# Kernel tuning notes

Hardware: AMD Instinct MI355X
Metric: run time of the kernel (lower is better)

The kernel has to match this reference:

```python
import jax, jax.numpy as jnp
import numpy as np

N_HEADS = 16


def _rotate_half(x):
    x_even = x[..., ::2]
    x_odd = x[..., 1::2]
    return jnp.stack((-x_odd, x_even), axis=-1).reshape(x.shape)


def _apply_rope(x, cos, sin):
    # cos/sin: (S, d_head) broadcast against (B, H, S, d_head)
    return x * cos + _rotate_half(x) * sin


def setup_inputs() -> dict:
    key = jax.random.key(0)
    k1, k2, k3 = jax.random.split(key, 3)
    B, S, D, H = 2, 2048, 1024, N_HEADS
    dh = D // H
    x = jax.random.normal(k1, (B, S, D), dtype=jnp.float32)
    w_qkv = jax.random.normal(k2, (D, 3 * D), dtype=jnp.float32) * 0.02
    w_proj = jax.random.normal(k3, (D, D), dtype=jnp.float32) * 0.02
    # standard interleaved RoPE tables, shape (S, d_head)
    inv_freq = 1.0 / (10000.0 ** (jnp.arange(0, dh, 2, dtype=jnp.float32) / dh))
    angles = jnp.arange(S, dtype=jnp.float32)[:, None] * inv_freq[None, :]  # (S, dh/2)
    rope_cos = jnp.repeat(jnp.cos(angles), 2, axis=-1)  # (S, dh)
    rope_sin = jnp.repeat(jnp.sin(angles), 2, axis=-1)
    return {"x": x, "w_qkv": w_qkv, "w_proj": w_proj, "rope_cos": rope_cos, "rope_sin": rope_sin}


def reference(x, w_qkv, w_proj, rope_cos, rope_sin):
    B, S, D = x.shape
    H = N_HEADS
    dh = D // H
    half = dh // 2
    qkv = x @ w_qkv  # (B, S, 3D)
    q, k, v = jnp.split(qkv, 3, axis=-1)
    # (B, S, D) -> (B, H, S, dh)
    q = q.reshape(B, S, H, dh).transpose(0, 2, 1, 3)
    k = k.reshape(B, S, H, dh).transpose(0, 2, 1, 3)
    v = v.reshape(B, S, H, dh).transpose(0, 2, 1, 3)
    q = _apply_rope(q, rope_cos, rope_sin)
    k = _apply_rope(k, rope_cos, rope_sin)
    scale = half ** -0.5
    # dual score matrices from the two half-subspaces
    attn_up = jnp.einsum('bhid,bhjd->bhij', q[..., :half], k[..., :half]) * scale
    attn_down = jnp.einsum('bhid,bhjd->bhij', q[..., half:], k[..., half:]) * scale
    lower_mask = jnp.tril(jnp.ones((S, S), dtype=bool))  # j <= i -> down
    attn_logits = jnp.where(lower_mask, attn_down, attn_up)
    attn_weights = jax.nn.softmax(attn_logits, axis=-1)
    attn_out = jnp.einsum('bhij,bhjd->bhid', attn_weights, v)
    attn_out = attn_out.transpose(0, 2, 1, 3).reshape(B, S, D)
    return attn_out @ w_proj
```

## Files before the change

### kernel.cpp

```cpp
#include <hip/hip_runtime.h>
#include <hip/hip_bf16.h>
#include <stdint.h>

typedef __bf16 bf16;
typedef __attribute__((ext_vector_type(4))) __bf16 bf16x4;
typedef __attribute__((ext_vector_type(8))) __bf16 bf16x8;
typedef __attribute__((ext_vector_type(4))) float f32x4;

#define MFMA16(a, b, c) __builtin_amdgcn_mfma_f32_16x16x32_bf16((a), (b), (c), 0, 0, 0)

#define QSC (0.17677669529663687f * 1.4426950408889634f)

__device__ __forceinline__ void async_cp16(const bf16* g, bf16* l) {
  __builtin_amdgcn_global_load_lds(
      (const __attribute__((address_space(1))) void*)g,
      (__attribute__((address_space(3))) void*)l, 16, 0, 0);
}

__global__ __launch_bounds__(256) void prep_k(const float* __restrict__ x,
                                              bf16* __restrict__ xb,
                                              const float* __restrict__ wqkv,
                                              bf16* __restrict__ wqkvT,
                                              const float* __restrict__ wproj,
                                              bf16* __restrict__ wprojT) {
  __shared__ bf16 t[64][65];
  const int bid = blockIdx.x;
  if (bid < 1024) {
    int i = (bid * 256 + threadIdx.x) * 4;
    const int stride = 1024 * 256 * 4;
    for (; i < 4194304; i += stride) {
      const f32x4 f = *(const f32x4*)(x + i);
      bf16x4 o;
      o[0] = (bf16)f[0]; o[1] = (bf16)f[1]; o[2] = (bf16)f[2]; o[3] = (bf16)f[3];
      *(bf16x4*)(xb + i) = o;
    }
    return;
  }
  const float* in;
  bf16* out;
  int R, C, tb;
  if (bid < 1792) { in = wqkv; out = wqkvT; R = 1024; C = 3072; tb = bid - 1024; }
  else            { in = wproj; out = wprojT; R = 1024; C = 1024; tb = bid - 1792; }
  const int tilesx = C >> 6;
  const int bc = (tb % tilesx) * 64, br = (tb / tilesx) * 64;
  const int tx = threadIdx.x & 63, ty = threadIdx.x >> 6;
#pragma unroll
  for (int r = ty; r < 64; r += 4) t[r][tx] = (bf16)in[(br + r) * C + bc + tx];
  __syncthreads();
#pragma unroll
  for (int r = ty; r < 64; r += 4) out[(bc + r) * R + br + tx] = t[tx][r];
}

template <int MODE, int BM>
__global__ __launch_bounds__(256) void gemm128(
    const bf16* __restrict__ A, const bf16* __restrict__ BT, int M, int N, int K,
    float* __restrict__ C, bf16* __restrict__ qws, bf16* __restrict__ kws,
    bf16* __restrict__ vT, const float* __restrict__ ropeC, const float* __restrict__ ropeS) {
  constexpr int MT = BM / 32;
  __shared__ __align__(16) bf16 As[BM * 64];
  __shared__ __align__(16) bf16 Bs[128 * 64];
  const int tid = threadIdx.x;
  const int lane = tid & 63, wave = tid >> 6;
  const int l16 = lane & 15, quad = lane >> 4;
  const int wm = (wave >> 1) * (BM / 2), wn = (wave & 1) * 64;
  const int bm = blockIdx.y, bn = blockIdx.x;

  const int srow = tid >> 3;
  const int schunk = ((tid & 7) - srow) & 7;
  const bf16* ag = A + (bm * BM + srow) * K + schunk * 8;
  const bf16* bg = BT + (bn * 128 + srow) * K + schunk * 8;
  bf16* la = &As[tid * 8];
  bf16* lb = &Bs[tid * 8];

  f32x4 acc[MT][4] = {};

  for (int k0 = 0; k0 < K; k0 += 64) {
    async_cp16(ag + k0, la);
    async_cp16(ag + 32 * K + k0, la + 2048);
    if (BM == 128) {
      async_cp16(ag + 64 * K + k0, la + 4096);
      async_cp16(ag + 96 * K + k0, la + 6144);
    }
    async_cp16(bg + k0, lb);
    async_cp16(bg + 32 * K + k0, lb + 2048);
    async_cp16(bg + 64 * K + k0, lb + 4096);
    async_cp16(bg + 96 * K + k0, lb + 6144);
    __syncthreads();
#pragma unroll
    for (int ks = 0; ks < 2; ++ks) {
      bf16x8 af[MT], bff[4];
#pragma unroll
      for (int t = 0; t < MT; ++t) {
        const int r = wm + t * 16 + l16;
        af[t] = *(const bf16x8*)&As[r * 64 + ((ks * 4 + quad + r) & 7) * 8];
      }
#pragma unroll
      for (int t = 0; t < 4; ++t) {
        const int r = wn + t * 16 + l16;
        bff[t] = *(const bf16x8*)&Bs[r * 64 + ((ks * 4 + quad + r) & 7) * 8];
      }
#pragma unroll
      for (int mt = 0; mt < MT; ++mt)
#pragma unroll
        for (int nt = 0; nt < 4; ++nt) acc[mt][nt] = MFMA16(af[mt], bff[nt], acc[mt][nt]);
    }
    __syncthreads();
  }

  if (MODE == 0) {
#pragma unroll
    for (int mt = 0; mt < MT; ++mt)
#pragma unroll
      for (int i = 0; i < 4; ++i) {
        const int row = bm * BM + wm + mt * 16 + quad * 4 + i;
#pragma unroll
        for (int nt = 0; nt < 4; ++nt) {
          const int col = bn * 128 + wn + nt * 16 + l16;
          C[row * N + col] = acc[mt][nt][i];
        }
      }
  } else {
    bf16* tb = &Bs[wave * 512];
#pragma unroll
    for (int mt = 0; mt < MT; ++mt) {
      const int s0 = bm * BM + wm + mt * 16;
      const int b = s0 >> 11, sbase = s0 & 2047;
#pragma unroll
      for (int nt = 0; nt < 4; ++nt) {
        const int colb = bn * 128 + wn + nt * 16;
        const int sec = colb >> 10, rem = colb & 1023;
        const int h = rem >> 6, d0 = rem & 63;
        if (sec < 2) {
          const int d = d0 + l16;
#pragma unroll
          for (int i = 0; i < 4; ++i) {
            const int s = sbase + quad * 4 + i;
            float v = acc[mt][nt][i];
            float pr = __shfl_xor(v, 1);
            float rot = (d & 1) ? pr : -pr;
            float rv = v * ropeC[s * 64 + d] + rot * ropeS[s * 64 + d];
            if (sec == 0) rv *= QSC;
            tb[(quad * 4 + i) * 20 + l16] = (bf16)rv;
          }
          bf16* dst = ((sec == 0) ? qws : kws) + ((b * 16 + h) * 2048 + sbase) * 64 + d0;
          bf16x4 seg = *(const bf16x4*)&tb[l16 * 20 + quad * 4];
          *(bf16x4*)(dst + l16 * 64 + quad * 4) = seg;
        } else {
          const int d = d0 + l16;
          const int s4 = sbase + quad * 4;
          const int a = (s4 >> 4) & 3;
          const int p = (s4 & ~63) | ((a >> 1) * 32 + quad * 8 + (a & 1) * 4);
          bf16x4 pk;
#pragma unroll
          for (int i = 0; i < 4; ++i) pk[i] = (bf16)acc[mt][nt][i];
          *(bf16x4*)(vT + ((b * 16 + h) * 64 + d) * 2048 + p) = pk;
        }
      }
    }
  }
}

template <int SPLIT>
__global__ __launch_bounds__(256) void attn_k(const bf16* __restrict__ qws,
                                              const bf16* __restrict__ kws,
                                              const bf16* __restrict__ vT,
                                              bf16* __restrict__ awA, bf16* __restrict__ pB,
                                              float* __restrict__ lA, float* __restrict__ lB) {
  __shared__ __align__(16) bf16 Ks[2][64 * 64];
  __shared__ __align__(16) bf16 Vs[2][64 * 64];
  const int tid = threadIdx.x;
  const int lane = tid & 63, wave = tid >> 6;
  const int l16 = lane & 15, quad = lane >> 4;
  int bh, qblk, kh;
  if (SPLIT) {
    bh = blockIdx.x & 31;
    const int q2 = blockIdx.x >> 5;
    qblk = q2 >> 1;
    kh = q2 & 1;
  } else {
    bh = blockIdx.x >> 4;
    qblk = blockIdx.x & 15;
    kh = 0;
  }
  const int b = bh >> 4, h = bh & 15;
  const int rbase = qblk * 128 + wave * 32;
  const int jt0 = kh * 16;
  const int jt1 = SPLIT ? jt0 + 16 : 32;

  const bf16* qb = qws + (bh * 2048 + rbase) * 64;
  const bf16* kb = kws + bh * 2048 * 64;
  const bf16* vb = vT + bh * 64 * 2048;

  const int r0 = wave * 16 + (lane >> 3);
  const int c0 = ((lane & 7) - r0) & 7;
  const bf16* kst0 = kb + r0 * 64 + c0 * 8;
  const bf16* kst1 = kb + (r0 + 8) * 64 + c0 * 8;
  const bf16* vst0 = vb + r0 * 2048 + c0 * 8;
  const bf16* vst1 = vb + (r0 + 8) * 2048 + c0 * 8;

#define STAGE(jtv)                                         \
  {                                                        \
    bf16* kdst = &Ks[(jtv) & 1][wave * 1024];              \
    bf16* vdst = &Vs[(jtv) & 1][wave * 1024];              \
    async_cp16(kst0 + (jtv) * 4096, kdst);                 \
    async_cp16(kst1 + (jtv) * 4096, kdst + 512);           \
    async_cp16(vst0 + (jtv) * 64, vdst);                   \
    async_cp16(vst1 + (jtv) * 64, vdst + 512);             \
  }

  bf16x8 qf[2][2];
#pragma unroll
  for (int g = 0; g < 2; ++g)
#pragma unroll
    for (int hf = 0; hf < 2; ++hf)
      qf[g][hf] = *(const bf16x8*)(qb + (g * 16 + l16) * 64 + hf * 32 + quad * 8);

  bf16x8 ones;
#pragma unroll
  for (int j = 0; j < 8; ++j) ones[j] = (bf16)1.0f;

  f32x4 o[2][4] = {};
  f32x4 o_l[2] = {};
  const f32x4 zz = {};
  const int tdw = rbase >> 6;

#define ATTN_BODY(TM, jt)                                                             \
  {                                                                                   \
    const bf16* Kb = Ks[(jt) & 1];                                                    \
    const bf16* Vb = Vs[(jt) & 1];                                                    \
    bf16x8 vf[2][4];                                                                  \
    _Pragma("unroll") for (int ks = 0; ks < 2; ++ks)                                  \
      _Pragma("unroll") for (int ntd = 0; ntd < 4; ++ntd)                             \
        vf[ks][ntd] = *(const bf16x8*)(Vb + (ntd * 16 + l16) * 64 +                   \
                                       ((ks * 4 + quad + l16) & 7) * 8);              \
    bf16x8 kfU[2][2], kfD[2][2];                                                      \
    _Pragma("unroll") for (int ks = 0; ks < 2; ++ks)                                  \
      _Pragma("unroll") for (int s = 0; s < 2; ++s) {                                 \
        const int ro = ((ks * 2 + s) * 16 + l16) * 64;                                \
        if (TM != 0) kfU[ks][s] = *(const bf16x8*)(Kb + ro + ((quad + l16) & 7) * 8); \
        if (TM != 2)                                                                  \
          kfD[ks][s] = *(const bf16x8*)(Kb + ro + ((4 + quad + l16) & 7) * 8);        \
      }                                                                               \
    if ((jt) + 1 < jt1) STAGE((jt) + 1)                                               \
    _Pragma("unroll") for (int ks = 0; ks < 2; ++ks) {                                \
      f32x4 sU[2][2], sD[2][2];                                                       \
      _Pragma("unroll") for (int s = 0; s < 2; ++s)                                   \
        _Pragma("unroll") for (int g = 0; g < 2; ++g) {                               \
          if (TM != 0) sU[s][g] = MFMA16(kfU[ks][s], qf[g][0], zz);                   \
          if (TM != 2) sD[s][g] = MFMA16(kfD[ks][s], qf[g][1], zz);                   \
        }                                                                             \
      _Pragma("unroll") for (int g = 0; g < 2; ++g) {                                 \
        bf16x8 af;                                                                    \
        _Pragma("unroll") for (int s = 0; s < 2; ++s)                                 \
          _Pragma("unroll") for (int r = 0; r < 4; ++r) {                             \
            float x;                                                                  \
            if (TM == 0) x = sD[s][g][r];                                             \
            else if (TM == 2) x = sU[s][g][r];                                        \
            else {                                                                    \
              const int jcol = (jt) * 64 + (ks * 2 + s) * 16 + quad * 4 + r;          \
              x = (jcol <= rbase + g * 16 + l16) ? sD[s][g][r] : sU[s][g][r];         \
            }                                                                         \
            af[s * 4 + r] = (bf16)__builtin_amdgcn_exp2f(x);                          \
          }                                                                           \
        o_l[g] = MFMA16(af, ones, o_l[g]);                                            \
        _Pragma("unroll") for (int ntd = 0; ntd < 4; ++ntd)                           \
            o[g][ntd] = MFMA16(af, vf[ks][ntd], o[g][ntd]);                           \
      }                                                                               \
    }                                                                                 \
  }

  STAGE(jt0)
  for (int jt = jt0; jt < jt1; ++jt) {
    asm volatile("s_waitcnt vmcnt(0)" ::: "memory");
    __syncthreads();
    if (jt < tdw) ATTN_BODY(0, jt)
    else if (jt == tdw) ATTN_BODY(1, jt)
    else ATTN_BODY(2, jt)
  }
#undef ATTN_BODY
#undef STAGE

  if (SPLIT) {
    bf16* p = kh ? pB : awA;
    float* lp = kh ? lB : lA;
#pragma unroll
    for (int g = 0; g < 2; ++g) {
#pragma unroll
      for (int ntd = 0; ntd < 4; ++ntd)
#pragma unroll
        for (int r = 0; r < 4; ++r)
          p[(b * 2048 + rbase + g * 16 + quad * 4 + r) * 1024 + h * 64 + ntd * 16 + l16] =
              (bf16)o[g][ntd][r];
      if (l16 == 0)
#pragma unroll
        for (int r = 0; r < 4; ++r)
          lp[bh * 2048 + rbase + g * 16 + quad * 4 + r] = o_l[g][r];
    }
  } else {
#pragma unroll
    for (int g = 0; g < 2; ++g) {
      float ir[4];
#pragma unroll
      for (int r = 0; r < 4; ++r) ir[r] = __builtin_amdgcn_rcpf(o_l[g][r]);
#pragma unroll
      for (int ntd = 0; ntd < 4; ++ntd)
#pragma unroll
        for (int r = 0; r < 4; ++r)
          awA[(b * 2048 + rbase + g * 16 + quad * 4 + r) * 1024 + h * 64 + ntd * 16 + l16] =
              (bf16)(o[g][ntd][r] * ir[r]);
    }
  }
}

__global__ __launch_bounds__(256) void merge_k(const bf16* __restrict__ pA,
                                               const bf16* __restrict__ pB,
                                               const float* __restrict__ lA,
                                               const float* __restrict__ lB,
                                               bf16* __restrict__ aw) {
  const int i = (blockIdx.x * 256 + threadIdx.x) * 4;
  const int rowg = i >> 10;
  const int col = i & 1023;
  const int b = rowg >> 11, s = rowg & 2047, h = col >> 6;
  const int bh = b * 16 + h;
  const float l = lA[bh * 2048 + s] + lB[bh * 2048 + s];
  const float ir = __builtin_amdgcn_rcpf(l);
  const bf16x4 a = *(const bf16x4*)(pA + i);
  const bf16x4 bb = *(const bf16x4*)(pB + i);
  bf16x4 o;
#pragma unroll
  for (int j = 0; j < 4; ++j) o[j] = (bf16)(((float)a[j] + (float)bb[j]) * ir);
  *(bf16x4*)(aw + i) = o;
}

extern "C" void kernel_launch(void* const* d_in, const int* in_sizes, int n_in,
                              void* d_out, int out_size, void* d_ws, size_t ws_size,
                              hipStream_t stream) {
  const float* x = (const float*)d_in[0];
  const float* w_qkv = (const float*)d_in[1];
  const float* w_proj = (const float*)d_in[2];
  const float* ropeC = (const float*)d_in[3];
  const float* ropeS = (const float*)d_in[4];
  float* out = (float*)d_out;

  char* ws = (char*)d_ws;
  bf16* xb = (bf16*)ws;     ws += (size_t)4194304 * 2;
  bf16* wqkvT = (bf16*)ws;  ws += (size_t)3145728 * 2;
  bf16* wprojT = (bf16*)ws; ws += (size_t)1048576 * 2;
  bf16* qws = (bf16*)ws;    ws += (size_t)4194304 * 2;
  bf16* kws = (bf16*)ws;    ws += (size_t)4194304 * 2;
  bf16* vT = (bf16*)ws;     ws += (size_t)4194304 * 2;
  bf16* aw = (bf16*)ws;     ws += (size_t)4194304 * 2;
  bf16* pA = (bf16*)ws;     ws += (size_t)4194304 * 2;
  bf16* pB = (bf16*)ws;     ws += (size_t)4194304 * 2;
  float* lA = (float*)ws;   ws += (size_t)65536 * 4;
  float* lB = (float*)ws;   ws += (size_t)65536 * 4;
  const size_t need_split = (size_t)(ws - (char*)d_ws);
  const bool use_split = ws_size >= need_split;

  prep_k<<<2048, 256, 0, stream>>>(x, xb, w_qkv, wqkvT, w_proj, wprojT);
  gemm128<1, 128><<<dim3(3072 / 128, 4096 / 128), 256, 0, stream>>>(
      xb, wqkvT, 4096, 3072, 1024, nullptr, qws, kws, vT, ropeC, ropeS);
  if (use_split) {
    attn_k<1><<<1024, 256, 0, stream>>>(qws, kws, vT, pA, pB, lA, lB);
    merge_k<<<4096, 256, 0, stream>>>(pA, pB, lA, lB, aw);
  } else {
    attn_k<0><<<512, 256, 0, stream>>>(qws, kws, vT, aw, nullptr, nullptr, nullptr);
  }
  gemm128<0, 64><<<dim3(1024 / 128, 4096 / 64), 256, 0, stream>>>(
      aw, wprojT, 4096, 1024, 1024, out, nullptr, nullptr, nullptr, nullptr, nullptr);
}
```

Before: 185.2 us.

## Double-buffer GEMM LDS tiles with K-step 32 and async prefetch

Restructures the bf16 GEMM main loop into a two-stage LDS pipeline. The K tile shrinks from 64 to 32 and the LDS swizzle changes to match. The next tile is issued with global_load_lds after the current fragments are read into registers, so the loads overlap with the MFMAs, and there is one barrier per iteration instead of two. The cost is twice as many loop iterations, each with a full vmcnt wait and a barrier. A barrier is added before the epilogue reuses the Bs buffer.

```diff
diff --git a/kernel.cpp b/kernel.cpp
--- a/kernel.cpp
+++ b/kernel.cpp
@@ -57,55 +57,56 @@
     float* __restrict__ C, bf16* __restrict__ qws, bf16* __restrict__ kws,
     bf16* __restrict__ vT, const float* __restrict__ ropeC, const float* __restrict__ ropeS) {
   constexpr int MT = BM / 32;
-  __shared__ __align__(16) bf16 As[BM * 64];
-  __shared__ __align__(16) bf16 Bs[128 * 64];
+  __shared__ __align__(16) bf16 As[2][BM * 32];
+  __shared__ __align__(16) bf16 Bs[2][128 * 32];
   const int tid = threadIdx.x;
   const int lane = tid & 63, wave = tid >> 6;
   const int l16 = lane & 15, quad = lane >> 4;
   const int wm = (wave >> 1) * (BM / 2), wn = (wave & 1) * 64;
   const int bm = blockIdx.y, bn = blockIdx.x;
 
-  const int srow = tid >> 3;
-  const int schunk = ((tid & 7) - srow) & 7;
+  const int srow = tid >> 2;
+  const int schunk = ((tid & 3) - (srow >> 1)) & 3;
   const bf16* ag = A + (bm * BM + srow) * K + schunk * 8;
   const bf16* bg = BT + (bn * 128 + srow) * K + schunk * 8;
-  bf16* la = &As[tid * 8];
-  bf16* lb = &Bs[tid * 8];
+
+#define GSTAGE(k0v, buf)                                        \
+  {                                                             \
+    bf16* la = &As[buf][tid * 8];                               \
+    bf16* lb = &Bs[buf][tid * 8];                               \
+    async_cp16(ag + (k0v), la);                                 \
+    if (BM == 128) async_cp16(ag + 64 * K + (k0v), la + 2048);  \
+    async_cp16(bg + (k0v), lb);                                 \
+    async_cp16(bg + 64 * K + (k0v), lb + 2048);                 \
+  }
 
   f32x4 acc[MT][4] = {};
-
-  for (int k0 = 0; k0 < K; k0 += 64) {
-    async_cp16(ag + k0, la);
-    async_cp16(ag + 32 * K + k0, la + 2048);
-    if (BM == 128) {
-      async_cp16(ag + 64 * K + k0, la + 4096);
-      async_cp16(ag + 96 * K + k0, la + 6144);
-    }
-    async_cp16(bg + k0, lb);
-    async_cp16(bg + 32 * K + k0, lb + 2048);
-    async_cp16(bg + 64 * K + k0, lb + 4096);
-    async_cp16(bg + 96 * K + k0, lb + 6144);
+  const int niter = K >> 5;
+
+  GSTAGE(0, 0)
+  for (int it = 0; it < niter; ++it) {
+    asm volatile("s_waitcnt vmcnt(0)" ::: "memory");
     __syncthreads();
-#pragma unroll
-    for (int ks = 0; ks < 2; ++ks) {
-      bf16x8 af[MT], bff[4];
-#pragma unroll
-      for (int t = 0; t < MT; ++t) {
-        const int r = wm + t * 16 + l16;
-        af[t] = *(const bf16x8*)&As[r * 64 + ((ks * 4 + quad + r) & 7) * 8];
-      }
-#pragma unroll
-      for (int t = 0; t < 4; ++t) {
-        const int r = wn + t * 16 + l16;
-        bff[t] = *(const bf16x8*)&Bs[r * 64 + ((ks * 4 + quad + r) & 7) * 8];
-      }
-#pragma unroll
-      for (int mt = 0; mt < MT; ++mt)
-#pragma unroll
-        for (int nt = 0; nt < 4; ++nt) acc[mt][nt] = MFMA16(af[mt], bff[nt], acc[mt][nt]);
-    }
-    __syncthreads();
-  }
+    const bf16* Ab = As[it & 1];
+    const bf16* Bb = Bs[it & 1];
+    bf16x8 af[MT], bff[4];
+#pragma unroll
+    for (int t = 0; t < MT; ++t) {
+      const int r = wm + t * 16 + l16;
+      af[t] = *(const bf16x8*)&Ab[r * 32 + ((((r >> 1) + quad) & 3) << 3)];
+    }
+#pragma unroll
+    for (int t = 0; t < 4; ++t) {
+      const int r = wn + t * 16 + l16;
+      bff[t] = *(const bf16x8*)&Bb[r * 32 + ((((r >> 1) + quad) & 3) << 3)];
+    }
+    if (it + 1 < niter) GSTAGE((it + 1) * 32, (it + 1) & 1)
+#pragma unroll
+    for (int mt = 0; mt < MT; ++mt)
+#pragma unroll
+      for (int nt = 0; nt < 4; ++nt) acc[mt][nt] = MFMA16(af[mt], bff[nt], acc[mt][nt]);
+  }
+#undef GSTAGE
 
   if (MODE == 0) {
 #pragma unroll
@@ -120,7 +121,8 @@
         }
       }
   } else {
-    bf16* tb = &Bs[wave * 512];
+    __syncthreads();
+    bf16* tb = &Bs[0][wave * 512];
 #pragma unroll
     for (int mt = 0; mt < MT; ++mt) {
       const int s0 = bm * BM + wm + mt * 16;
```

Measured after the change: 182.8 us. About the same (-1.3%).
